# Performance work log

Hardware: AMD Instinct MI355X
Metric: run time of the kernel (lower is better)

The kernel has to match this reference:

```python
import jax, jax.numpy as jnp
import numpy as np

BIN_SIZE = 128
DIST_MULT = 0.1
LN_EPS = 1e-6


def setup_inputs() -> dict:
    key = jax.random.key(0)
    ks = jax.random.split(key, 24)
    B, N, D, DD, H = 8, 25600, 256, 128, 128
    s = 0.02
    inp = {
        'x': jax.random.normal(ks[0], (B, N, D), dtype=jnp.float32),
        'msk': jax.random.randint(ks[1], (B, N), 0, 2) > 0,
        'ln_g': jnp.ones((D,), jnp.float32),
        'ln_b': jnp.zeros((D,), jnp.float32),
        # ffn_dist: Linear(256,128) ELU Linear(128,128) ELU Linear(128,128)
        'w1': s * jax.random.normal(ks[2], (D, H), jnp.float32),
        'b1': jnp.zeros((H,), jnp.float32),
        'w2': s * jax.random.normal(ks[3], (H, H), jnp.float32),
        'b2': jnp.zeros((H,), jnp.float32),
        'w3': s * jax.random.normal(ks[4], (H, DD), jnp.float32),
        'b3': jnp.zeros((DD,), jnp.float32),
        # LSH codebook random rotations [distance_dim, max_num_bins//2]
        'codebook': jax.random.normal(ks[5], (DD, 100), jnp.float32),
        # two GHConvDense layers, hidden_dim=output_dim=256
        'theta0': jax.random.normal(ks[6], (D, D), jnp.float32) * s,
        'wh0': jax.random.normal(ks[7], (D, D), jnp.float32) * s,
        'wt0': jax.random.normal(ks[8], (D, D), jnp.float32) * s,
        'bt0': jnp.zeros((D,), jnp.float32),
        'theta1': jax.random.normal(ks[9], (D, D), jnp.float32) * s,
        'wh1': jax.random.normal(ks[10], (D, D), jnp.float32) * s,
        'wt1': jax.random.normal(ks[11], (D, D), jnp.float32) * s,
        'bt1': jnp.zeros((D,), jnp.float32),
    }
    return inp


def _forward(x, msk, ln_g, ln_b, w1, b1, w2, b2, w3, b3, codebook,
             theta0, wh0, wt0, bt0, theta1, wh1, wt1, bt1):
    B, n_elems, D = x.shape
    pad = (-n_elems) % BIN_SIZE  # static python int
    if pad:
        x = jnp.pad(x, ((0, 0), (0, pad), (0, 0)))
        msk = jnp.pad(msk, ((0, 0), (0, pad)), constant_values=True)
    Np = n_elems + pad
    n_bins = Np // BIN_SIZE

    # layernorm
    mu = jnp.mean(x, -1, keepdims=True)
    var = jnp.mean(jnp.square(x - mu), -1, keepdims=True)
    xn = (x - mu) * jax.lax.rsqrt(var + LN_EPS) * ln_g + ln_b

    # distance FFN + dist activation (elu)
    h = jax.nn.elu(xn @ w1 + b1)
    h = jax.nn.elu(h @ w2 + b2)
    x_dist = jax.nn.elu(h @ w3 + b3)  # [B, Np, distance_dim]

    # LSH binning
    mul = x_dist @ codebook[:, :max(1, n_bins // 2)]
    cmul = jnp.concatenate([mul, -mul], axis=-1)  # [B, Np, n_bins]
    a = jnp.argmax(cmul, axis=-1)
    bin_idx = a + jnp.where(msk, 0, n_bins - 1)
    bins_split = jnp.argsort(bin_idx, axis=-1)  # [B, Np]

    # gather into bins
    xm = jnp.take_along_axis(x_dist, bins_split[..., None], axis=1)
    xm = xm.reshape(B, n_bins, BIN_SIZE, x_dist.shape[-1])
    xb = jnp.take_along_axis(xn, bins_split[..., None], axis=1)
    xb = xb.reshape(B, n_bins, BIN_SIZE, D)
    mskf = jnp.take_along_axis(msk, bins_split, axis=1)
    mskf = mskf.reshape(B, n_bins, BIN_SIZE, 1).astype(x.dtype)

    # pairwise Gaussian kernel within each bin
    xk = xm * mskf
    nsq = jnp.sum(jnp.square(xk), -1)  # [B, nb, P]
    inner = jnp.einsum('bnpd,bnqd->bnpq', xk, xk)
    d2 = nsq[..., :, None] - 2.0 * inner + nsq[..., None, :]
    dist = jnp.sqrt(jnp.clip(d2, 1e-6, 1e6))
    dm = jnp.clip(jnp.exp(-DIST_MULT * dist), 0.0, 1.0)
    dm = dm * mskf * jnp.swapaxes(mskf, -1, -2)  # mask rows & cols [B,nb,P,P]

    # gated graph convolutions
    for th, wh, wt, bt in ((theta0, wh0, wt0, bt0), (theta1, wh1, wt1, bt1)):
        xmk = xb * mskf
        f_hom = jnp.einsum('bnpq,bnqd->bnpd', dm, (xmk @ th) * mskf)
        f_het = xmk @ wh
        gate = jax.nn.sigmoid(xb @ wt + bt)
        xb = jax.nn.elu(gate * f_hom + (1.0 - gate) * f_het) * mskf

    # reverse LSH scatter
    xb_flat = xb.reshape(B, Np, D)
    ret = jax.vmap(lambda idx, pts: jnp.zeros((Np, D), pts.dtype).at[idx].set(pts))(
        bins_split, xb_flat)
    return ret[:, :n_elems, :]


def reference(x, msk, ln_g, ln_b, w1, b1, w2, b2, w3, b3, codebook,
              theta0, wh0, wt0, bt0, theta1, wh1, wt1, bt1):
    return _forward(x, msk, ln_g, ln_b, w1, b1, w2, b2, w3, b3, codebook,
                    theta0, wh0, wt0, bt0, theta1, wh1, wt1, bt1)
```

## Files before the change

kernel.cpp:

```cpp
#include <hip/hip_runtime.h>
#include <math.h>

#define B_ 8
#define NP_ 25600
#define T_ (B_*NP_)
#define D_ 256
#define H_ 128
#define DD_ 128
#define NBINS_ 200
#define NIDS_ 400
#define PB_ 128
#define NC_ 100
#define GT_ (B_*NBINS_)

typedef __attribute__((ext_vector_type(8))) short bf16x8;
typedef __attribute__((ext_vector_type(4))) float f32x4;
typedef __attribute__((ext_vector_type(4))) unsigned short u16x4;
typedef unsigned short u16;

__device__ __forceinline__ float eluf(float v){ return v > 0.f ? v : expm1f(v); }
__device__ __forceinline__ u16 f2bf(float f){
  union { float f; unsigned u; } v; v.f = f;
  unsigned r = v.u + 0x7fffu + ((v.u >> 16) & 1u);
  return (u16)(r >> 16);
}
__device__ __forceinline__ float bf2f(u16 h){
  union { unsigned u; float f; } v; v.u = ((unsigned)h) << 16; return v.f;
}

__global__ void k_mask_detect(const unsigned int* __restrict__ m, int* __restrict__ flags){
  int any_f1 = 0, any_o = 0;
  for (int i = blockIdx.x*blockDim.x + threadIdx.x; i < T_/4; i += gridDim.x*blockDim.x){
    unsigned int w = m[i];
    if (w == 0x3F800000u) any_f1 = 1;
    else if (w > 1u) any_o = 1;
  }
  if (any_f1) atomicOr(&flags[0], 1);
  if (any_o)  atomicOr(&flags[1], 1);
}

__global__ void k_mask_convert(const void* __restrict__ m, const int* __restrict__ flags,
                               float* __restrict__ mskf){
  int i = blockIdx.x*256 + threadIdx.x;
  int mode = flags[0] ? 2 : (flags[1] ? 1 : 0);
  bool v;
  if (mode == 2)      v = ((const float*)m)[i] != 0.f;
  else if (mode == 1) v = ((const unsigned char*)m)[i] != 0;
  else                v = ((const int*)m)[i] != 0;
  mskf[i] = v ? 1.f : 0.f;
}

__global__ __launch_bounds__(256) void k_ln(const float* __restrict__ x,
    const float* __restrict__ g, const float* __restrict__ b, float* __restrict__ xn){
  const int wave = threadIdx.x >> 6, lane = threadIdx.x & 63;
  const long t = (long)blockIdx.x*4 + wave;
  float4 v = ((const float4*)(x + t*D_))[lane];
  float s  = v.x + v.y + v.z + v.w;
  float s2 = v.x*v.x + v.y*v.y + v.z*v.z + v.w*v.w;
  #pragma unroll
  for (int o = 32; o; o >>= 1){ s += __shfl_xor(s, o); s2 += __shfl_xor(s2, o); }
  const float mu = s * (1.f/D_);
  float var = s2*(1.f/D_) - mu*mu;
  var = fmaxf(var, 0.f);
  const float rs = rsqrtf(var + 1e-6f);
  float4 gg = ((const float4*)g)[lane];
  float4 bb = ((const float4*)b)[lane];
  float4 o4;
  o4.x = (v.x-mu)*rs*gg.x + bb.x;
  o4.y = (v.y-mu)*rs*gg.y + bb.y;
  o4.z = (v.z-mu)*rs*gg.z + bb.z;
  o4.w = (v.w-mu)*rs*gg.w + bb.w;
  ((float4*)(xn + t*D_))[lane] = o4;
}

template<int K>
__global__ __launch_bounds__(256) void k_gemm2(const float* __restrict__ A,
    const float* __restrict__ W, const float* __restrict__ bias, float* __restrict__ C){
  __shared__ __align__(16) float As[32*132];
  __shared__ __align__(16) float Bs[32*132];
  const size_t m0 = (size_t)blockIdx.x * 128;
  const int tid = threadIdx.x;
  const int tm = tid >> 4, tn = tid & 15;
  float acc[8][8] = {};
  for (int kc = 0; kc < K; kc += 32){
    __syncthreads();
    {
      const int r = tid >> 1, kq = (tid & 1) * 16;
      const float* src = &A[(m0 + r)*(size_t)K + kc + kq];
      #pragma unroll
      for (int q = 0; q < 4; ++q){
        const float4 v = ((const float4*)src)[q];
        As[(kq + q*4 + 0)*132 + r] = v.x;
        As[(kq + q*4 + 1)*132 + r] = v.y;
        As[(kq + q*4 + 2)*132 + r] = v.z;
        As[(kq + q*4 + 3)*132 + r] = v.w;
      }
      const int kk = tid >> 3, n0 = (tid & 7) * 16;
      const float* wsrc = &W[(size_t)(kc + kk)*128 + n0];
      #pragma unroll
      for (int q = 0; q < 4; ++q)
        *(float4*)&Bs[kk*132 + n0 + q*4] = ((const float4*)wsrc)[q];
    }
    __syncthreads();
    #pragma unroll
    for (int k = 0; k < 32; ++k){
      float a[8], b[8];
      *(float4*)&a[0] = *(const float4*)&As[k*132 + tm*8];
      *(float4*)&a[4] = *(const float4*)&As[k*132 + tm*8 + 4];
      *(float4*)&b[0] = *(const float4*)&Bs[k*132 + tn*8];
      *(float4*)&b[4] = *(const float4*)&Bs[k*132 + tn*8 + 4];
      #pragma unroll
      for (int i = 0; i < 8; ++i)
        #pragma unroll
        for (int j = 0; j < 8; ++j)
          acc[i][j] = fmaf(a[i], b[j], acc[i][j]);
    }
  }
  #pragma unroll
  for (int i = 0; i < 8; ++i){
    const size_t row = m0 + tm*8 + i;
    #pragma unroll
    for (int q = 0; q < 2; ++q){
      float4 o;
      o.x = eluf(acc[i][q*4+0] + bias[tn*8 + q*4+0]);
      o.y = eluf(acc[i][q*4+1] + bias[tn*8 + q*4+1]);
      o.z = eluf(acc[i][q*4+2] + bias[tn*8 + q*4+2]);
      o.w = eluf(acc[i][q*4+3] + bias[tn*8 + q*4+3]);
      *(float4*)&C[row*128 + tn*8 + q*4] = o;
    }
  }
}

__global__ void k_cbpad(const float* __restrict__ cb, float* __restrict__ cbp){
  const int k = blockIdx.x, c = threadIdx.x;
  cbp[k*128 + c] = (c < NC_) ? cb[k*NC_ + c] : 0.f;
}

__global__ __launch_bounds__(256) void k_mulmax(const float* __restrict__ A,
    const float* __restrict__ CB, const float* __restrict__ mskf, int* __restrict__ bidx){
  __shared__ __align__(16) float As[32*132];
  __shared__ __align__(16) float Bs[32*132];
  const size_t m0 = (size_t)blockIdx.x * 128;
  const int tid = threadIdx.x;
  const int tm = tid >> 4, tn = tid & 15;
  float acc[8][8] = {};
  for (int kc = 0; kc < DD_; kc += 32){
    __syncthreads();
    {
      const int r = tid >> 1, kq = (tid & 1) * 16;
      const float* src = &A[(m0 + r)*(size_t)DD_ + kc + kq];
      #pragma unroll
      for (int q = 0; q < 4; ++q){
        const float4 v = ((const float4*)src)[q];
        As[(kq + q*4 + 0)*132 + r] = v.x;
        As[(kq + q*4 + 1)*132 + r] = v.y;
        As[(kq + q*4 + 2)*132 + r] = v.z;
        As[(kq + q*4 + 3)*132 + r] = v.w;
      }
      const int kk = tid >> 3, n0 = (tid & 7) * 16;
      const float* wsrc = &CB[(size_t)(kc + kk)*128 + n0];
      #pragma unroll
      for (int q = 0; q < 4; ++q)
        *(float4*)&Bs[kk*132 + n0 + q*4] = ((const float4*)wsrc)[q];
    }
    __syncthreads();
    #pragma unroll
    for (int k = 0; k < 32; ++k){
      float a[8], b[8];
      *(float4*)&a[0] = *(const float4*)&As[k*132 + tm*8];
      *(float4*)&a[4] = *(const float4*)&As[k*132 + tm*8 + 4];
      *(float4*)&b[0] = *(const float4*)&Bs[k*132 + tn*8];
      *(float4*)&b[4] = *(const float4*)&Bs[k*132 + tn*8 + 4];
      #pragma unroll
      for (int i = 0; i < 8; ++i)
        #pragma unroll
        for (int j = 0; j < 8; ++j)
          acc[i][j] = fmaf(a[i], b[j], acc[i][j]);
    }
  }
  #pragma unroll
  for (int i = 0; i < 8; ++i){
    float bv = -1e30f; int bi = 0;
    #pragma unroll
    for (int j = 0; j < 8; ++j){
      const int c = tn*8 + j;
      if (c < NC_){
        const float v = acc[i][j];
        if (v > bv || (v == bv && c < bi)){ bv = v; bi = c; }
        const float nv = -v; const int nc2 = c + NC_;
        if (nv > bv || (nv == bv && nc2 < bi)){ bv = nv; bi = nc2; }
      }
    }
    #pragma unroll
    for (int o = 1; o < 16; o <<= 1){
      const float ov = __shfl_xor(bv, o);
      const int oi = __shfl_xor(bi, o);
      if (ov > bv || (ov == bv && oi < bi)){ bv = ov; bi = oi; }
    }
    if (tn == 0){
      const size_t t = m0 + tm*8 + i;
      bidx[t] = bi + (mskf[t] != 0.f ? 0 : NBINS_ - 1);
    }
  }
}

__global__ void k_hist(const int* __restrict__ bidx, int* __restrict__ hist){
  const int i = blockIdx.x*256 + threadIdx.x;
  const int b = i / NP_;
  atomicAdd(&hist[b*NIDS_ + bidx[i]], 1);
}

__global__ void k_prefix(const int* __restrict__ hist, int* __restrict__ offs){
  const int b = threadIdx.x;
  if (b < B_){
    int run = 0;
    for (int v = 0; v < NIDS_; ++v){ offs[b*NIDS_ + v] = run; run += hist[b*NIDS_ + v]; }
  }
}

__global__ __launch_bounds__(64) void k_binsort(const int* __restrict__ bidx,
    const int* __restrict__ offs, const int* __restrict__ hist, int* __restrict__ split){
  const int bv = blockIdx.x;
  if (hist[bv] == 0) return;
  const int b = bv / NIDS_, v = bv % NIDS_;
  int base = offs[bv];
  const int lane = threadIdx.x;
  const int* row = bidx + b*NP_;
  for (int i0 = 0; i0 < NP_; i0 += 64){
    const int i = i0 + lane;
    const bool m = (row[i] == v);
    const unsigned long long mk = __ballot(m);
    if (m){
      const int pos = base + __popcll(mk & ((1ull << lane) - 1ull));
      split[b*NP_ + pos] = i;
    }
    base += __popcll(mk);
  }
}

__global__ __launch_bounds__(256) void k_gather(const float* __restrict__ xn,
    const float* __restrict__ xd, const float* __restrict__ mskf,
    const int* __restrict__ split, u16* __restrict__ xmh,
    u16* __restrict__ xkh, float* __restrict__ mskg){
  const long j = (long)blockIdx.x*4 + (threadIdx.x >> 6);
  const int lane = threadIdx.x & 63;
  const int b = (int)(j / NP_);
  const int i = split[j];
  const long src = (long)b*NP_ + i;
  const float mv = mskf[src];
  const float4 v = ((const float4*)(xn + src*D_))[lane];
  u16x4 o;
  o[0] = f2bf(v.x*mv); o[1] = f2bf(v.y*mv); o[2] = f2bf(v.z*mv); o[3] = f2bf(v.w*mv);
  ((u16x4*)(xmh + j*D_))[lane] = o;
  if (lane < 32){
    const float4 w = ((const float4*)(xd + src*DD_))[lane];
    u16x4 ow;
    ow[0] = f2bf(w.x*mv); ow[1] = f2bf(w.y*mv); ow[2] = f2bf(w.z*mv); ow[3] = f2bf(w.w*mv);
    ((u16x4*)(xkh + j*DD_))[lane] = ow;
  }
  if (lane == 0) mskg[j] = mv;
}

__global__ __launch_bounds__(256) void k_wt(const float* __restrict__ W, u16* __restrict__ o){
  const int n = blockIdx.x, k = threadIdx.x;
  o[n*D_ + k] = f2bf(W[k*D_ + n]);
}
__global__ __launch_bounds__(256) void k_wt2(const float* __restrict__ wt,
    const float* __restrict__ wh, u16* __restrict__ o){
  const int n = blockIdx.x, k = threadIdx.x;
  const float v = (n < 256) ? wt[(size_t)k*D_ + n] : wh[(size_t)k*D_ + (n-256)];
  o[(size_t)n*D_ + k] = f2bf(v);
}

__device__ __forceinline__ void stage64(const u16* __restrict__ g, size_t row0,
    int ld, int k0, u16* Ls, int tid){
  #pragma unroll
  for (int s = 0; s < 4; ++s){
    const int r = (tid >> 3) + s*32, c8 = tid & 7;
    bf16x8 v = *(const bf16x8*)&g[(row0 + r)*(size_t)ld + k0 + c8*8];
    *(bf16x8*)&Ls[(r*8 + (c8 ^ (r & 7)))*8] = v;
  }
}
__device__ __forceinline__ void stage128(const u16* __restrict__ g, size_t row0,
    int ld, u16* Ls, int tid){
  #pragma unroll
  for (int s = 0; s < 8; ++s){
    const int r = (tid >> 4) + s*16, c8 = tid & 15;
    bf16x8 v = *(const bf16x8*)&g[(row0 + r)*(size_t)ld + c8*8];
    *(bf16x8*)&Ls[(r*16 + (c8 ^ (r & 7)))*8] = v;
  }
}
__device__ __forceinline__ bf16x8 ldf(const u16* Ls, int row, int c8, int ldc8){
  return *(const bf16x8*)&Ls[(row*ldc8 + (c8 ^ (row & 7)))*8];
}

__global__ __launch_bounds__(256) void k_dm(const u16* __restrict__ xk,
    const float* __restrict__ rm, u16* __restrict__ dmb){
  __shared__ __align__(16) u16 Xs[128*128];
  __shared__ float nsq[128];
  __shared__ float msl[128];
  const int g = blockIdx.x;
  const int tid = threadIdx.x, l = tid & 63, wid = tid >> 6;
  const int wr = wid >> 1, wc = wid & 1, lm = l & 15, lk = l >> 4;
  stage128(xk, (size_t)g*128, DD_, Xs, tid);
  if (tid < 128) msl[tid] = rm[(size_t)g*128 + tid];
  __syncthreads();
  f32x4 acc[4][4] = {};
  #pragma unroll
  for (int ks = 0; ks < 4; ++ks){
    bf16x8 a[4], b[4];
    #pragma unroll
    for (int mi = 0; mi < 4; ++mi) a[mi] = ldf(Xs, wr*64 + mi*16 + lm, ks*4 + lk, 16);
    #pragma unroll
    for (int ni = 0; ni < 4; ++ni) b[ni] = ldf(Xs, wc*64 + ni*16 + lm, ks*4 + lk, 16);
    #pragma unroll
    for (int mi = 0; mi < 4; ++mi)
      #pragma unroll
      for (int ni = 0; ni < 4; ++ni)
        acc[mi][ni] = __builtin_amdgcn_mfma_f32_16x16x32_bf16(a[mi], b[ni], acc[mi][ni], 0, 0, 0);
  }
  if (wr == wc && ((lm >> 2) == lk)){
    #pragma unroll
    for (int mi = 0; mi < 4; ++mi)
      nsq[wr*64 + mi*16 + lm] = acc[mi][mi][lm & 3];
  }
  __syncthreads();
  #pragma unroll
  for (int mi = 0; mi < 4; ++mi)
    #pragma unroll
    for (int ni = 0; ni < 4; ++ni)
      #pragma unroll
      for (int r = 0; r < 4; ++r){
        const int row = wr*64 + mi*16 + lk*4 + r;
        const int col = wc*64 + ni*16 + lm;
        float d2 = nsq[row] + nsq[col] - 2.f*acc[mi][ni][r];
        d2 = fminf(fmaxf(d2, 1e-6f), 1e6f);
        float w = expf(-0.1f * sqrtf(d2));
        w = fminf(w, 1.f);
        dmb[((size_t)g*PB_ + row)*PB_ + col] = f2bf(w * msl[row] * msl[col]);
      }
}

__global__ __launch_bounds__(256) void k_tmm(const u16* __restrict__ thT,
    const u16* __restrict__ X, u16* __restrict__ tT){
  __shared__ __align__(16) u16 As[128*64];
  __shared__ __align__(16) u16 Bs[128*64];
  const int g = blockIdx.x, h = blockIdx.y;
  const int tid = threadIdx.x, l = tid & 63, wid = tid >> 6;
  const int wr = wid >> 1, wc = wid & 1, lm = l & 15, lk = l >> 4;
  f32x4 acc[4][4] = {};
  for (int kt = 0; kt < 4; ++kt){
    if (kt) __syncthreads();
    stage64(thT, (size_t)h*128, D_, kt*64, As, tid);
    stage64(X,   (size_t)g*128, D_, kt*64, Bs, tid);
    __syncthreads();
    #pragma unroll
    for (int ks = 0; ks < 2; ++ks){
      bf16x8 a[4], b[4];
      #pragma unroll
      for (int mi = 0; mi < 4; ++mi) a[mi] = ldf(As, wr*64 + mi*16 + lm, ks*4 + lk, 8);
      #pragma unroll
      for (int ni = 0; ni < 4; ++ni) b[ni] = ldf(Bs, wc*64 + ni*16 + lm, ks*4 + lk, 8);
      #pragma unroll
      for (int mi = 0; mi < 4; ++mi)
        #pragma unroll
        for (int ni = 0; ni < 4; ++ni)
          acc[mi][ni] = __builtin_amdgcn_mfma_f32_16x16x32_bf16(a[mi], b[ni], acc[mi][ni], 0, 0, 0);
    }
  }
  #pragma unroll
  for (int mi = 0; mi < 4; ++mi)
    #pragma unroll
    for (int ni = 0; ni < 4; ++ni)
      #pragma unroll
      for (int r = 0; r < 4; ++r){
        const int row = wr*64 + mi*16 + lk*4 + r;
        const int col = wc*64 + ni*16 + lm;
        tT[((size_t)g*D_ + h*128 + row)*PB_ + col] = f2bf(acc[mi][ni][r]);
      }
}

__global__ __launch_bounds__(256) void k_gg(const u16* __restrict__ X,
    const u16* __restrict__ WT, u16* __restrict__ o){
  __shared__ __align__(16) u16 As[128*64];
  __shared__ __align__(16) u16 Bs[128*64];
  const int n0 = blockIdx.x * 128;
  const size_t r0 = (size_t)blockIdx.y * 128;
  const int tid = threadIdx.x, l = tid & 63, wid = tid >> 6;
  const int wr = wid >> 1, wc = wid & 1, lm = l & 15, lk = l >> 4;
  f32x4 acc[4][4] = {};
  for (int kt = 0; kt < 4; ++kt){
    if (kt) __syncthreads();
    stage64(X,  r0,          D_, kt*64, As, tid);
    stage64(WT, (size_t)n0,  D_, kt*64, Bs, tid);
    __syncthreads();
    #pragma unroll
    for (int ks = 0; ks < 2; ++ks){
      bf16x8 a[4], b[4];
      #pragma unroll
      for (int mi = 0; mi < 4; ++mi) a[mi] = ldf(As, wr*64 + mi*16 + lm, ks*4 + lk, 8);
      #pragma unroll
      for (int ni = 0; ni < 4; ++ni) b[ni] = ldf(Bs, wc*64 + ni*16 + lm, ks*4 + lk, 8);
      #pragma unroll
      for (int mi = 0; mi < 4; ++mi)
        #pragma unroll
        for (int ni = 0; ni < 4; ++ni)
          acc[mi][ni] = __builtin_amdgcn_mfma_f32_16x16x32_bf16(a[mi], b[ni], acc[mi][ni], 0, 0, 0);
    }
  }
  #pragma unroll
  for (int mi = 0; mi < 4; ++mi)
    #pragma unroll
    for (int ni = 0; ni < 4; ++ni)
      #pragma unroll
      for (int r = 0; r < 4; ++r){
        const int row = wr*64 + mi*16 + lk*4 + r;
        const int col = wc*64 + ni*16 + lm;
        o[(r0 + row)*512 + n0 + col] = f2bf(acc[mi][ni][r]);
      }
}

template<int OUT>
__global__ __launch_bounds__(256) void k_bmix(const u16* __restrict__ dmb,
    const u16* __restrict__ tT, const u16* __restrict__ atah,
    const float* __restrict__ btv, const int* __restrict__ split,
    u16* __restrict__ o16, float* __restrict__ o32){
  __shared__ __align__(16) u16 As[128*128];
  __shared__ __align__(16) u16 Bs[128*128];
  __shared__ int ssp[128];
  const int h = blockIdx.x, g = blockIdx.y;
  const int tid = threadIdx.x, l = tid & 63, wid = tid >> 6;
  const int wr = wid >> 1, wc = wid & 1, lm = l & 15, lk = l >> 4;
  stage128(dmb, (size_t)g*128, PB_, As, tid);
  stage128(tT, (size_t)g*D_ + h*128, PB_, Bs, tid);
  if (OUT){ if (tid < 128) ssp[tid] = split[g*128 + tid]; }
  __syncthreads();
  f32x4 acc[4][4] = {};
  #pragma unroll
  for (int ks = 0; ks < 4; ++ks){
    bf16x8 a[4], b[4];
    #pragma unroll
    for (int mi = 0; mi < 4; ++mi) a[mi] = ldf(As, wr*64 + mi*16 + lm, ks*4 + lk, 16);
    #pragma unroll
    for (int ni = 0; ni < 4; ++ni) b[ni] = ldf(Bs, wc*64 + ni*16 + lm, ks*4 + lk, 16);
    #pragma unroll
    for (int mi = 0; mi < 4; ++mi)
      #pragma unroll
      for (int ni = 0; ni < 4; ++ni)
        acc[mi][ni] = __builtin_amdgcn_mfma_f32_16x16x32_bf16(a[mi], b[ni], acc[mi][ni], 0, 0, 0);
  }
  __syncthreads();
  #pragma unroll
  for (int s = 0; s < 8; ++s){
    const int r = (tid >> 4) + s*16, c8 = tid & 15;
    const size_t gbase = ((size_t)g*128 + r)*512 + h*128 + c8*8;
    *(bf16x8*)&As[r*128 + c8*8] = *(const bf16x8*)&atah[gbase];
    *(bf16x8*)&Bs[r*128 + c8*8] = *(const bf16x8*)&atah[gbase + 256];
  }
  __syncthreads();
  #pragma unroll
  for (int mi = 0; mi < 4; ++mi)
    #pragma unroll
    for (int ni = 0; ni < 4; ++ni){
      const int colc = wc*64 + ni*16 + lm;
      const int gc = h*128 + colc;
      const float bb = btv[gc];
      #pragma unroll
      for (int r = 0; r < 4; ++r){
        const int row = wr*64 + mi*16 + lk*4 + r;
        const float at = bf2f(As[row*128 + colc]);
        const float ahv = bf2f(Bs[row*128 + colc]);
        const float gt = 1.f/(1.f + expf(-(at + bb)));
        const float o = eluf(gt*acc[mi][ni][r] + (1.f - gt)*ahv);
        if (OUT == 0){
          o16[((size_t)g*128 + row)*D_ + gc] = f2bf(o);
        } else {
          const int b = g / NBINS_;
          o32[((size_t)b*NP_ + ssp[row])*D_ + gc] = o;
        }
      }
    }
}

extern "C" void kernel_launch(void* const* d_in, const int* in_sizes, int n_in,
                              void* d_out, int out_size, void* d_ws, size_t ws_size,
                              hipStream_t stream){
  (void)in_sizes; (void)n_in; (void)out_size;
  const float* x    = (const float*)d_in[0];
  const void*  msk  = d_in[1];
  const float* ln_g = (const float*)d_in[2];
  const float* ln_b = (const float*)d_in[3];
  const float* w1 = (const float*)d_in[4];
  const float* b1 = (const float*)d_in[5];
  const float* w2 = (const float*)d_in[6];
  const float* b2 = (const float*)d_in[7];
  const float* w3 = (const float*)d_in[8];
  const float* b3 = (const float*)d_in[9];
  const float* cb = (const float*)d_in[10];
  const float* th0 = (const float*)d_in[11];
  const float* wh0 = (const float*)d_in[12];
  const float* wt0 = (const float*)d_in[13];
  const float* bt0 = (const float*)d_in[14];
  const float* th1 = (const float*)d_in[15];
  const float* wh1 = (const float*)d_in[16];
  const float* wt1 = (const float*)d_in[17];
  const float* bt1 = (const float*)d_in[18];
  float* out = (float*)d_out;

  char* ws = (char*)d_ws;
  size_t off = 0;
  auto alloc = [&](size_t bytes) -> void* {
    void* p = ws + off; off += (bytes + 255) & ~(size_t)255; return p;
  };
  int* flags = (int*)alloc(2*sizeof(int));
  int* hist  = (int*)alloc((size_t)B_*NIDS_*4);
  int* offs  = (int*)alloc((size_t)B_*NIDS_*4);
  int* bidx  = (int*)alloc((size_t)T_*4);
  int* split = (int*)alloc((size_t)T_*4);
  float* mskf = (float*)alloc((size_t)T_*4);
  float* mskg = (float*)alloc((size_t)T_*4);
  float* cbp = (float*)alloc((size_t)128*128*4);
  u16* thT0 = (u16*)alloc((size_t)D_*D_*2);
  u16* thT1 = (u16*)alloc((size_t)D_*D_*2);
  u16* wtwh0 = (u16*)alloc((size_t)512*D_*2);
  u16* wtwh1 = (u16*)alloc((size_t)512*D_*2);
  char* regA = (char*)alloc((size_t)T_*512*2);
  u16* xmh = (u16*)alloc((size_t)T_*D_*2);
  char* regC = (char*)alloc((size_t)T_*D_*2);
  u16* tT  = (u16*)alloc((size_t)T_*D_*2);
  u16* xb1 = (u16*)alloc((size_t)T_*D_*2);
  if (off > ws_size) return;

  float* P = (float*)regA;
  float* Q = P + (size_t)T_*DD_;
  u16* atah = (u16*)regA;
  u16* xkh = (u16*)regC;
  u16* dmb = xkh + (size_t)T_*DD_;
  float* xn = out;

  hipMemsetAsync(flags, 0, 2*sizeof(int), stream);
  hipMemsetAsync(hist, 0, (size_t)B_*NIDS_*4, stream);

  k_mask_detect<<<64, 256, 0, stream>>>((const unsigned int*)msk, flags);
  k_mask_convert<<<T_/256, 256, 0, stream>>>(msk, flags, mskf);

  k_ln<<<T_/4, 256, 0, stream>>>(x, ln_g, ln_b, xn);

  k_cbpad<<<128, 128, 0, stream>>>(cb, cbp);
  k_wt<<<256, 256, 0, stream>>>(th0, thT0);
  k_wt<<<256, 256, 0, stream>>>(th1, thT1);
  k_wt2<<<512, 256, 0, stream>>>(wt0, wh0, wtwh0);
  k_wt2<<<512, 256, 0, stream>>>(wt1, wh1, wtwh1);

  k_gemm2<D_><<<T_/128, 256, 0, stream>>>(xn, w1, b1, P);
  k_gemm2<H_><<<T_/128, 256, 0, stream>>>(P, w2, b2, Q);
  k_gemm2<H_><<<T_/128, 256, 0, stream>>>(Q, w3, b3, P);

  k_mulmax<<<T_/128, 256, 0, stream>>>(P, cbp, mskf, bidx);
  k_hist<<<T_/256, 256, 0, stream>>>(bidx, hist);
  k_prefix<<<1, 64, 0, stream>>>(hist, offs);
  k_binsort<<<B_*NIDS_, 64, 0, stream>>>(bidx, offs, hist, split);

  k_gather<<<T_/4, 256, 0, stream>>>(xn, P, mskf, split, xmh, xkh, mskg);
  k_dm<<<GT_, 256, 0, stream>>>(xkh, mskg, dmb);

  k_gg<<<dim3(4, T_/128), 256, 0, stream>>>(xmh, wtwh0, atah);
  k_tmm<<<dim3(GT_, 2), 256, 0, stream>>>(thT0, xmh, tT);
  k_bmix<0><<<dim3(2, GT_), 256, 0, stream>>>(dmb, tT, atah, bt0, nullptr, xb1, nullptr);

  k_gg<<<dim3(4, T_/128), 256, 0, stream>>>(xb1, wtwh1, atah);
  k_tmm<<<dim3(GT_, 2), 256, 0, stream>>>(thT1, xb1, tT);
  k_bmix<1><<<dim3(2, GT_), 256, 0, stream>>>(dmb, tT, atah, bt1, split, nullptr, out);
}
```

Before: 1.524 ms.

## Stage GEMM tiles with direct global-to-LDS loads and register-prefetch A tiles

Replaces register round-trip staging of shared-memory tiles with global_load_lds direct copies across the bf16 MFMA kernels and the fp32 GEMMs, keeping the XOR swizzle by permuting source addresses instead of destination slots. In the fp32 GEMM and codebook kernels, the A tile is prefetched into registers one k-chunk ahead so the global load overlaps the FMA loop, and the B tile loses its padding. This is meant to cut VGPR pressure and load-store instruction count during staging. The risk is that the unpadded B layout causes LDS bank conflicts and that the direct loads need correct waits before the barrier.

```diff
diff --git a/kernel.cpp b/kernel.cpp
--- a/kernel.cpp
+++ b/kernel.cpp
@@ -26,6 +26,11 @@
 }
 __device__ __forceinline__ float bf2f(u16 h){
   union { unsigned u; float f; } v; v.u = ((unsigned)h) << 16; return v.f;
+}
+
+__device__ __forceinline__ void gl16(void* lds, const void* g){
+  __builtin_amdgcn_global_load_lds((const __attribute__((address_space(1))) void*)g,
+                                   (__attribute__((address_space(3))) void*)lds, 16, 0, 0);
 }
 
 __global__ void k_mask_detect(const unsigned int* __restrict__ m, int* __restrict__ flags){
@@ -77,38 +82,47 @@
 __global__ __launch_bounds__(256) void k_gemm2(const float* __restrict__ A,
     const float* __restrict__ W, const float* __restrict__ bias, float* __restrict__ C){
   __shared__ __align__(16) float As[32*132];
-  __shared__ __align__(16) float Bs[32*132];
+  __shared__ __align__(16) float Bs[32*128];
   const size_t m0 = (size_t)blockIdx.x * 128;
   const int tid = threadIdx.x;
   const int tm = tid >> 4, tn = tid & 15;
+  const int w = tid >> 6, l = tid & 63;
+  const int ar = tid >> 1, akq = (tid & 1) * 16;
   float acc[8][8] = {};
+  float4 pre[4];
+  {
+    const float* src = &A[(m0 + ar)*(size_t)K + akq];
+    #pragma unroll
+    for (int q = 0; q < 4; ++q) pre[q] = ((const float4*)src)[q];
+  }
   for (int kc = 0; kc < K; kc += 32){
+    if (kc) __syncthreads();
+    #pragma unroll
+    for (int q = 0; q < 4; ++q){
+      As[(akq + q*4 + 0)*132 + ar] = pre[q].x;
+      As[(akq + q*4 + 1)*132 + ar] = pre[q].y;
+      As[(akq + q*4 + 2)*132 + ar] = pre[q].z;
+      As[(akq + q*4 + 3)*132 + ar] = pre[q].w;
+    }
+    #pragma unroll
+    for (int s = 0; s < 4; ++s){
+      const int G = (s*4 + w)*64 + l;
+      const int r = G >> 5, c4 = G & 31;
+      gl16(&Bs[G*4], &W[(size_t)(kc + r)*128 + c4*4]);
+    }
     __syncthreads();
-    {
-      const int r = tid >> 1, kq = (tid & 1) * 16;
-      const float* src = &A[(m0 + r)*(size_t)K + kc + kq];
-      #pragma unroll
-      for (int q = 0; q < 4; ++q){
-        const float4 v = ((const float4*)src)[q];
-        As[(kq + q*4 + 0)*132 + r] = v.x;
-        As[(kq + q*4 + 1)*132 + r] = v.y;
-        As[(kq + q*4 + 2)*132 + r] = v.z;
-        As[(kq + q*4 + 3)*132 + r] = v.w;
-      }
-      const int kk = tid >> 3, n0 = (tid & 7) * 16;
-      const float* wsrc = &W[(size_t)(kc + kk)*128 + n0];
-      #pragma unroll
-      for (int q = 0; q < 4; ++q)
-        *(float4*)&Bs[kk*132 + n0 + q*4] = ((const float4*)wsrc)[q];
-    }
-    __syncthreads();
+    if (kc + 32 < K){
+      const float* src = &A[(m0 + ar)*(size_t)K + kc + 32 + akq];
+      #pragma unroll
+      for (int q = 0; q < 4; ++q) pre[q] = ((const float4*)src)[q];
+    }
     #pragma unroll
     for (int k = 0; k < 32; ++k){
       float a[8], b[8];
       *(float4*)&a[0] = *(const float4*)&As[k*132 + tm*8];
       *(float4*)&a[4] = *(const float4*)&As[k*132 + tm*8 + 4];
-      *(float4*)&b[0] = *(const float4*)&Bs[k*132 + tn*8];
-      *(float4*)&b[4] = *(const float4*)&Bs[k*132 + tn*8 + 4];
+      *(float4*)&b[0] = *(const float4*)&Bs[k*128 + tn*8];
+      *(float4*)&b[4] = *(const float4*)&Bs[k*128 + tn*8 + 4];
       #pragma unroll
       for (int i = 0; i < 8; ++i)
         #pragma unroll
@@ -139,38 +153,47 @@
 __global__ __launch_bounds__(256) void k_mulmax(const float* __restrict__ A,
     const float* __restrict__ CB, const float* __restrict__ mskf, int* __restrict__ bidx){
   __shared__ __align__(16) float As[32*132];
-  __shared__ __align__(16) float Bs[32*132];
+  __shared__ __align__(16) float Bs[32*128];
   const size_t m0 = (size_t)blockIdx.x * 128;
   const int tid = threadIdx.x;
   const int tm = tid >> 4, tn = tid & 15;
+  const int w = tid >> 6, l = tid & 63;
+  const int ar = tid >> 1, akq = (tid & 1) * 16;
   float acc[8][8] = {};
+  float4 pre[4];
+  {
+    const float* src = &A[(m0 + ar)*(size_t)DD_ + akq];
+    #pragma unroll
+    for (int q = 0; q < 4; ++q) pre[q] = ((const float4*)src)[q];
+  }
   for (int kc = 0; kc < DD_; kc += 32){
+    if (kc) __syncthreads();
+    #pragma unroll
+    for (int q = 0; q < 4; ++q){
+      As[(akq + q*4 + 0)*132 + ar] = pre[q].x;
+      As[(akq + q*4 + 1)*132 + ar] = pre[q].y;
+      As[(akq + q*4 + 2)*132 + ar] = pre[q].z;
+      As[(akq + q*4 + 3)*132 + ar] = pre[q].w;
+    }
+    #pragma unroll
+    for (int s = 0; s < 4; ++s){
+      const int G = (s*4 + w)*64 + l;
+      const int r = G >> 5, c4 = G & 31;
+      gl16(&Bs[G*4], &CB[(size_t)(kc + r)*128 + c4*4]);
+    }
     __syncthreads();
-    {
-      const int r = tid >> 1, kq = (tid & 1) * 16;
-      const float* src = &A[(m0 + r)*(size_t)DD_ + kc + kq];
-      #pragma unroll
-      for (int q = 0; q < 4; ++q){
-        const float4 v = ((const float4*)src)[q];
-        As[(kq + q*4 + 0)*132 + r] = v.x;
-        As[(kq + q*4 + 1)*132 + r] = v.y;
-        As[(kq + q*4 + 2)*132 + r] = v.z;
-        As[(kq + q*4 + 3)*132 + r] = v.w;
-      }
-      const int kk = tid >> 3, n0 = (tid & 7) * 16;
-      const float* wsrc = &CB[(size_t)(kc + kk)*128 + n0];
-      #pragma unroll
-      for (int q = 0; q < 4; ++q)
-        *(float4*)&Bs[kk*132 + n0 + q*4] = ((const float4*)wsrc)[q];
-    }
-    __syncthreads();
+    if (kc + 32 < DD_){
+      const float* src = &A[(m0 + ar)*(size_t)DD_ + kc + 32 + akq];
+      #pragma unroll
+      for (int q = 0; q < 4; ++q) pre[q] = ((const float4*)src)[q];
+    }
     #pragma unroll
     for (int k = 0; k < 32; ++k){
       float a[8], b[8];
       *(float4*)&a[0] = *(const float4*)&As[k*132 + tm*8];
       *(float4*)&a[4] = *(const float4*)&As[k*132 + tm*8 + 4];
-      *(float4*)&b[0] = *(const float4*)&Bs[k*132 + tn*8];
-      *(float4*)&b[4] = *(const float4*)&Bs[k*132 + tn*8 + 4];
+      *(float4*)&b[0] = *(const float4*)&Bs[k*128 + tn*8];
+      *(float4*)&b[4] = *(const float4*)&Bs[k*128 + tn*8 + 4];
       #pragma unroll
       for (int i = 0; i < 8; ++i)
         #pragma unroll
@@ -253,9 +276,9 @@
   o[0] = f2bf(v.x*mv); o[1] = f2bf(v.y*mv); o[2] = f2bf(v.z*mv); o[3] = f2bf(v.w*mv);
   ((u16x4*)(xmh + j*D_))[lane] = o;
   if (lane < 32){
-    const float4 w = ((const float4*)(xd + src*DD_))[lane];
+    const float4 ww = ((const float4*)(xd + src*DD_))[lane];
     u16x4 ow;
-    ow[0] = f2bf(w.x*mv); ow[1] = f2bf(w.y*mv); ow[2] = f2bf(w.z*mv); ow[3] = f2bf(w.w*mv);
+    ow[0] = f2bf(ww.x*mv); ow[1] = f2bf(ww.y*mv); ow[2] = f2bf(ww.z*mv); ow[3] = f2bf(ww.w*mv);
     ((u16x4*)(xkh + j*DD_))[lane] = ow;
   }
   if (lane == 0) mskg[j] = mv;
@@ -272,22 +295,24 @@
   o[(size_t)n*D_ + k] = f2bf(v);
 }
 
-__device__ __forceinline__ void stage64(const u16* __restrict__ g, size_t row0,
+__device__ __forceinline__ void stage64a(const u16* __restrict__ g, size_t row0,
     int ld, int k0, u16* Ls, int tid){
+  const int w = tid >> 6, l = tid & 63;
   #pragma unroll
   for (int s = 0; s < 4; ++s){
-    const int r = (tid >> 3) + s*32, c8 = tid & 7;
-    bf16x8 v = *(const bf16x8*)&g[(row0 + r)*(size_t)ld + k0 + c8*8];
-    *(bf16x8*)&Ls[(r*8 + (c8 ^ (r & 7)))*8] = v;
-  }
-}
-__device__ __forceinline__ void stage128(const u16* __restrict__ g, size_t row0,
+    const int G = (s*4 + w)*64 + l;
+    const int r = G >> 3, c8 = G & 7;
+    gl16(&Ls[G*8], &g[(row0 + r)*(size_t)ld + k0 + ((c8 ^ (r & 7))*8)]);
+  }
+}
+__device__ __forceinline__ void stage128a(const u16* __restrict__ g, size_t row0,
     int ld, u16* Ls, int tid){
+  const int w = tid >> 6, l = tid & 63;
   #pragma unroll
   for (int s = 0; s < 8; ++s){
-    const int r = (tid >> 4) + s*16, c8 = tid & 15;
-    bf16x8 v = *(const bf16x8*)&g[(row0 + r)*(size_t)ld + c8*8];
-    *(bf16x8*)&Ls[(r*16 + (c8 ^ (r & 7)))*8] = v;
+    const int G = (s*4 + w)*64 + l;
+    const int r = G >> 4, c8 = G & 15;
+    gl16(&Ls[G*8], &g[(row0 + r)*(size_t)ld + ((c8 ^ (r & 7))*8)]);
   }
 }
 __device__ __forceinline__ bf16x8 ldf(const u16* Ls, int row, int c8, int ldc8){
@@ -302,7 +327,7 @@
   const int g = blockIdx.x;
   const int tid = threadIdx.x, l = tid & 63, wid = tid >> 6;
   const int wr = wid >> 1, wc = wid & 1, lm = l & 15, lk = l >> 4;
-  stage128(xk, (size_t)g*128, DD_, Xs, tid);
+  stage128a(xk, (size_t)g*128, DD_, Xs, tid);
   if (tid < 128) msl[tid] = rm[(size_t)g*128 + tid];
   __syncthreads();
   f32x4 acc[4][4] = {};
@@ -351,8 +376,8 @@
   f32x4 acc[4][4] = {};
   for (int kt = 0; kt < 4; ++kt){
     if (kt) __syncthreads();
-    stage64(thT, (size_t)h*128, D_, kt*64, As, tid);
-    stage64(X,   (size_t)g*128, D_, kt*64, Bs, tid);
+    stage64a(thT, (size_t)h*128, D_, kt*64, As, tid);
+    stage64a(X,   (size_t)g*128, D_, kt*64, Bs, tid);
     __syncthreads();
     #pragma unroll
     for (int ks = 0; ks < 2; ++ks){
@@ -391,8 +416,8 @@
   f32x4 acc[4][4] = {};
   for (int kt = 0; kt < 4; ++kt){
     if (kt) __syncthreads();
-    stage64(X,  r0,          D_, kt*64, As, tid);
-    stage64(WT, (size_t)n0,  D_, kt*64, Bs, tid);
+    stage64a(X,  r0,          D_, kt*64, As, tid);
+    stage64a(WT, (size_t)n0,  D_, kt*64, Bs, tid);
     __syncthreads();
     #pragma unroll
     for (int ks = 0; ks < 2; ++ks){
@@ -431,8 +456,8 @@
   const int h = blockIdx.x, g = blockIdx.y;
   const int tid = threadIdx.x, l = tid & 63, wid = tid >> 6;
   const int wr = wid >> 1, wc = wid & 1, lm = l & 15, lk = l >> 4;
-  stage128(dmb, (size_t)g*128, PB_, As, tid);
-  stage128(tT, (size_t)g*D_ + h*128, PB_, Bs, tid);
+  stage128a(dmb, (size_t)g*128, PB_, As, tid);
+  stage128a(tT, (size_t)g*D_ + h*128, PB_, Bs, tid);
   if (OUT){ if (tid < 128) ssp[tid] = split[g*128 + tid]; }
   __syncthreads();
   f32x4 acc[4][4] = {};
@@ -450,12 +475,16 @@
         acc[mi][ni] = __builtin_amdgcn_mfma_f32_16x16x32_bf16(a[mi], b[ni], acc[mi][ni], 0, 0, 0);
   }
   __syncthreads();
-  #pragma unroll
-  for (int s = 0; s < 8; ++s){
-    const int r = (tid >> 4) + s*16, c8 = tid & 15;
-    const size_t gbase = ((size_t)g*128 + r)*512 + h*128 + c8*8;
-    *(bf16x8*)&As[r*128 + c8*8] = *(const bf16x8*)&atah[gbase];
-    *(bf16x8*)&Bs[r*128 + c8*8] = *(const bf16x8*)&atah[gbase + 256];
+  {
+    const int w = tid >> 6, ll = tid & 63;
+    #pragma unroll
+    for (int s = 0; s < 8; ++s){
+      const int G = (s*4 + w)*64 + ll;
+      const int r = G >> 4, c8 = G & 15;
+      const size_t gbase = ((size_t)g*128 + r)*512 + h*128 + c8*8;
+      gl16(&As[G*8], &atah[gbase]);
+      gl16(&Bs[G*8], &atah[gbase + 256]);
+    }
   }
   __syncthreads();
   #pragma unroll
```

After: 1.556 ms. 2.1% more time.

## Fuse theta GEMM into bin-mix kernel and stage tiles via direct global-to-LDS loads

Applied to the files above, without the earlier changes.

Removes the separate k_tmm kernel and its tT intermediate. Each k_tbmix block now computes its 128x128 slice of theta^T·X in registers, writes it swizzled into LDS, and immediately multiplies by the distance matrix. This eliminates a full write and read of a T×256 bf16 buffer and two launches. Separately, tile staging now uses global_load_lds, with the XOR swizzle moved to the global address side, so data skips the register round trip. In exchange, the fused kernel does more serial work per block and uses more LDS.

```diff
diff --git a/kernel.cpp b/kernel.cpp
--- a/kernel.cpp
+++ b/kernel.cpp
@@ -26,6 +26,11 @@
 }
 __device__ __forceinline__ float bf2f(u16 h){
   union { unsigned u; float f; } v; v.u = ((unsigned)h) << 16; return v.f;
+}
+
+__device__ __forceinline__ void gl16(void* lds, const void* g){
+  __builtin_amdgcn_global_load_lds((const __attribute__((address_space(1))) void*)g,
+                                   (__attribute__((address_space(3))) void*)lds, 16, 0, 0);
 }
 
 __global__ void k_mask_detect(const unsigned int* __restrict__ m, int* __restrict__ flags){
@@ -253,9 +258,9 @@
   o[0] = f2bf(v.x*mv); o[1] = f2bf(v.y*mv); o[2] = f2bf(v.z*mv); o[3] = f2bf(v.w*mv);
   ((u16x4*)(xmh + j*D_))[lane] = o;
   if (lane < 32){
-    const float4 w = ((const float4*)(xd + src*DD_))[lane];
+    const float4 ww = ((const float4*)(xd + src*DD_))[lane];
     u16x4 ow;
-    ow[0] = f2bf(w.x*mv); ow[1] = f2bf(w.y*mv); ow[2] = f2bf(w.z*mv); ow[3] = f2bf(w.w*mv);
+    ow[0] = f2bf(ww.x*mv); ow[1] = f2bf(ww.y*mv); ow[2] = f2bf(ww.z*mv); ow[3] = f2bf(ww.w*mv);
     ((u16x4*)(xkh + j*DD_))[lane] = ow;
   }
   if (lane == 0) mskg[j] = mv;
@@ -272,22 +277,24 @@
   o[(size_t)n*D_ + k] = f2bf(v);
 }
 
-__device__ __forceinline__ void stage64(const u16* __restrict__ g, size_t row0,
+__device__ __forceinline__ void stage64a(const u16* __restrict__ g, size_t row0,
     int ld, int k0, u16* Ls, int tid){
+  const int w = tid >> 6, l = tid & 63;
   #pragma unroll
   for (int s = 0; s < 4; ++s){
-    const int r = (tid >> 3) + s*32, c8 = tid & 7;
-    bf16x8 v = *(const bf16x8*)&g[(row0 + r)*(size_t)ld + k0 + c8*8];
-    *(bf16x8*)&Ls[(r*8 + (c8 ^ (r & 7)))*8] = v;
-  }
-}
-__device__ __forceinline__ void stage128(const u16* __restrict__ g, size_t row0,
+    const int G = (s*4 + w)*64 + l;
+    const int r = G >> 3, c8 = G & 7;
+    gl16(&Ls[G*8], &g[(row0 + r)*(size_t)ld + k0 + ((c8 ^ (r & 7))*8)]);
+  }
+}
+__device__ __forceinline__ void stage128a(const u16* __restrict__ g, size_t row0,
     int ld, u16* Ls, int tid){
+  const int w = tid >> 6, l = tid & 63;
   #pragma unroll
   for (int s = 0; s < 8; ++s){
-    const int r = (tid >> 4) + s*16, c8 = tid & 15;
-    bf16x8 v = *(const bf16x8*)&g[(row0 + r)*(size_t)ld + c8*8];
-    *(bf16x8*)&Ls[(r*16 + (c8 ^ (r & 7)))*8] = v;
+    const int G = (s*4 + w)*64 + l;
+    const int r = G >> 4, c8 = G & 15;
+    gl16(&Ls[G*8], &g[(row0 + r)*(size_t)ld + ((c8 ^ (r & 7))*8)]);
   }
 }
 __device__ __forceinline__ bf16x8 ldf(const u16* Ls, int row, int c8, int ldc8){
@@ -302,7 +309,7 @@
   const int g = blockIdx.x;
   const int tid = threadIdx.x, l = tid & 63, wid = tid >> 6;
   const int wr = wid >> 1, wc = wid & 1, lm = l & 15, lk = l >> 4;
-  stage128(xk, (size_t)g*128, DD_, Xs, tid);
+  stage128a(xk, (size_t)g*128, DD_, Xs, tid);
   if (tid < 128) msl[tid] = rm[(size_t)g*128 + tid];
   __syncthreads();
   f32x4 acc[4][4] = {};
@@ -338,45 +345,6 @@
         float w = expf(-0.1f * sqrtf(d2));
         w = fminf(w, 1.f);
         dmb[((size_t)g*PB_ + row)*PB_ + col] = f2bf(w * msl[row] * msl[col]);
-      }
-}
-
-__global__ __launch_bounds__(256) void k_tmm(const u16* __restrict__ thT,
-    const u16* __restrict__ X, u16* __restrict__ tT){
-  __shared__ __align__(16) u16 As[128*64];
-  __shared__ __align__(16) u16 Bs[128*64];
-  const int g = blockIdx.x, h = blockIdx.y;
-  const int tid = threadIdx.x, l = tid & 63, wid = tid >> 6;
-  const int wr = wid >> 1, wc = wid & 1, lm = l & 15, lk = l >> 4;
-  f32x4 acc[4][4] = {};
-  for (int kt = 0; kt < 4; ++kt){
-    if (kt) __syncthreads();
-    stage64(thT, (size_t)h*128, D_, kt*64, As, tid);
-    stage64(X,   (size_t)g*128, D_, kt*64, Bs, tid);
-    __syncthreads();
-    #pragma unroll
-    for (int ks = 0; ks < 2; ++ks){
-      bf16x8 a[4], b[4];
-      #pragma unroll
-      for (int mi = 0; mi < 4; ++mi) a[mi] = ldf(As, wr*64 + mi*16 + lm, ks*4 + lk, 8);
-      #pragma unroll
-      for (int ni = 0; ni < 4; ++ni) b[ni] = ldf(Bs, wc*64 + ni*16 + lm, ks*4 + lk, 8);
-      #pragma unroll
-      for (int mi = 0; mi < 4; ++mi)
-        #pragma unroll
-        for (int ni = 0; ni < 4; ++ni)
-          acc[mi][ni] = __builtin_amdgcn_mfma_f32_16x16x32_bf16(a[mi], b[ni], acc[mi][ni], 0, 0, 0);
-    }
-  }
-  #pragma unroll
-  for (int mi = 0; mi < 4; ++mi)
-    #pragma unroll
-    for (int ni = 0; ni < 4; ++ni)
-      #pragma unroll
-      for (int r = 0; r < 4; ++r){
-        const int row = wr*64 + mi*16 + lk*4 + r;
-        const int col = wc*64 + ni*16 + lm;
-        tT[((size_t)g*D_ + h*128 + row)*PB_ + col] = f2bf(acc[mi][ni][r]);
       }
 }
 
@@ -391,8 +359,8 @@
   f32x4 acc[4][4] = {};
   for (int kt = 0; kt < 4; ++kt){
     if (kt) __syncthreads();
-    stage64(X,  r0,          D_, kt*64, As, tid);
-    stage64(WT, (size_t)n0,  D_, kt*64, Bs, tid);
+    stage64a(X,  r0,          D_, kt*64, As, tid);
+    stage64a(WT, (size_t)n0,  D_, kt*64, Bs, tid);
     __syncthreads();
     #pragma unroll
     for (int ks = 0; ks < 2; ++ks){
@@ -421,28 +389,60 @@
 }
 
 template<int OUT>
-__global__ __launch_bounds__(256) void k_bmix(const u16* __restrict__ dmb,
-    const u16* __restrict__ tT, const u16* __restrict__ atah,
-    const float* __restrict__ btv, const int* __restrict__ split,
-    u16* __restrict__ o16, float* __restrict__ o32){
-  __shared__ __align__(16) u16 As[128*128];
-  __shared__ __align__(16) u16 Bs[128*128];
+__global__ __launch_bounds__(256) void k_tbmix(const u16* __restrict__ dmb,
+    const u16* __restrict__ thT, const u16* __restrict__ X,
+    const u16* __restrict__ atah, const float* __restrict__ btv,
+    const int* __restrict__ split, u16* __restrict__ o16, float* __restrict__ o32){
+  __shared__ __align__(16) u16 bufA[128*128];
+  __shared__ __align__(16) u16 bufB[128*128];
   __shared__ int ssp[128];
   const int h = blockIdx.x, g = blockIdx.y;
   const int tid = threadIdx.x, l = tid & 63, wid = tid >> 6;
   const int wr = wid >> 1, wc = wid & 1, lm = l & 15, lk = l >> 4;
-  stage128(dmb, (size_t)g*128, PB_, As, tid);
-  stage128(tT, (size_t)g*D_ + h*128, PB_, Bs, tid);
+  u16* SA = bufA;
+  u16* SB = bufA + 128*64;
   if (OUT){ if (tid < 128) ssp[tid] = split[g*128 + tid]; }
+  f32x4 acc1[4][4] = {};
+  for (int kt = 0; kt < 4; ++kt){
+    if (kt) __syncthreads();
+    stage64a(thT, (size_t)h*128, D_, kt*64, SA, tid);
+    stage64a(X,   (size_t)g*128, D_, kt*64, SB, tid);
+    __syncthreads();
+    #pragma unroll
+    for (int ks = 0; ks < 2; ++ks){
+      bf16x8 a[4], b[4];
+      #pragma unroll
+      for (int mi = 0; mi < 4; ++mi) a[mi] = ldf(SA, wr*64 + mi*16 + lm, ks*4 + lk, 8);
+      #pragma unroll
+      for (int ni = 0; ni < 4; ++ni) b[ni] = ldf(SB, wc*64 + ni*16 + lm, ks*4 + lk, 8);
+      #pragma unroll
+      for (int mi = 0; mi < 4; ++mi)
+        #pragma unroll
+        for (int ni = 0; ni < 4; ++ni)
+          acc1[mi][ni] = __builtin_amdgcn_mfma_f32_16x16x32_bf16(a[mi], b[ni], acc1[mi][ni], 0, 0, 0);
+    }
+  }
+  __syncthreads();
+  #pragma unroll
+  for (int mi = 0; mi < 4; ++mi)
+    #pragma unroll
+    for (int ni = 0; ni < 4; ++ni)
+      #pragma unroll
+      for (int r = 0; r < 4; ++r){
+        const int row = wr*64 + mi*16 + lk*4 + r;
+        const int col = wc*64 + ni*16 + lm;
+        bufB[(row*16 + ((col >> 3) ^ (row & 7)))*8 + (col & 7)] = f2bf(acc1[mi][ni][r]);
+      }
+  stage128a(dmb, (size_t)g*128, PB_, bufA, tid);
   __syncthreads();
   f32x4 acc[4][4] = {};
   #pragma unroll
   for (int ks = 0; ks < 4; ++ks){
     bf16x8 a[4], b[4];
     #pragma unroll
-    for (int mi = 0; mi < 4; ++mi) a[mi] = ldf(As, wr*64 + mi*16 + lm, ks*4 + lk, 16);
-    #pragma unroll
-    for (int ni = 0; ni < 4; ++ni) b[ni] = ldf(Bs, wc*64 + ni*16 + lm, ks*4 + lk, 16);
+    for (int mi = 0; mi < 4; ++mi) a[mi] = ldf(bufA, wr*64 + mi*16 + lm, ks*4 + lk, 16);
+    #pragma unroll
+    for (int ni = 0; ni < 4; ++ni) b[ni] = ldf(bufB, wc*64 + ni*16 + lm, ks*4 + lk, 16);
     #pragma unroll
     for (int mi = 0; mi < 4; ++mi)
       #pragma unroll
@@ -450,12 +450,16 @@
         acc[mi][ni] = __builtin_amdgcn_mfma_f32_16x16x32_bf16(a[mi], b[ni], acc[mi][ni], 0, 0, 0);
   }
   __syncthreads();
-  #pragma unroll
-  for (int s = 0; s < 8; ++s){
-    const int r = (tid >> 4) + s*16, c8 = tid & 15;
-    const size_t gbase = ((size_t)g*128 + r)*512 + h*128 + c8*8;
-    *(bf16x8*)&As[r*128 + c8*8] = *(const bf16x8*)&atah[gbase];
-    *(bf16x8*)&Bs[r*128 + c8*8] = *(const bf16x8*)&atah[gbase + 256];
+  {
+    const int w = tid >> 6, ll = tid & 63;
+    #pragma unroll
+    for (int s = 0; s < 8; ++s){
+      const int G = (s*4 + w)*64 + ll;
+      const int r = G >> 4, c8 = G & 15;
+      const size_t gbase = ((size_t)g*128 + r)*512 + h*128 + c8*8;
+      gl16(&bufA[G*8], &atah[gbase]);
+      gl16(&bufB[G*8], &atah[gbase + 256]);
+    }
   }
   __syncthreads();
   #pragma unroll
@@ -468,8 +472,8 @@
       #pragma unroll
       for (int r = 0; r < 4; ++r){
         const int row = wr*64 + mi*16 + lk*4 + r;
-        const float at = bf2f(As[row*128 + colc]);
-        const float ahv = bf2f(Bs[row*128 + colc]);
+        const float at = bf2f(bufA[row*128 + colc]);
+        const float ahv = bf2f(bufB[row*128 + colc]);
         const float gt = 1.f/(1.f + expf(-(at + bb)));
         const float o = eluf(gt*acc[mi][ni][r] + (1.f - gt)*ahv);
         if (OUT == 0){
@@ -527,7 +531,6 @@
   char* regA = (char*)alloc((size_t)T_*512*2);
   u16* xmh = (u16*)alloc((size_t)T_*D_*2);
   char* regC = (char*)alloc((size_t)T_*D_*2);
-  u16* tT  = (u16*)alloc((size_t)T_*D_*2);
   u16* xb1 = (u16*)alloc((size_t)T_*D_*2);
   if (off > ws_size) return;
 
@@ -565,10 +568,8 @@
   k_dm<<<GT_, 256, 0, stream>>>(xkh, mskg, dmb);
 
   k_gg<<<dim3(4, T_/128), 256, 0, stream>>>(xmh, wtwh0, atah);
-  k_tmm<<<dim3(GT_, 2), 256, 0, stream>>>(thT0, xmh, tT);
-  k_bmix<0><<<dim3(2, GT_), 256, 0, stream>>>(dmb, tT, atah, bt0, nullptr, xb1, nullptr);
+  k_tbmix<0><<<dim3(2, GT_), 256, 0, stream>>>(dmb, thT0, xmh, atah, bt0, nullptr, xb1, nullptr);
 
   k_gg<<<dim3(4, T_/128), 256, 0, stream>>>(xb1, wtwh1, atah);
-  k_tmm<<<dim3(GT_, 2), 256, 0, stream>>>(thT1, xb1, tT);
-  k_bmix<1><<<dim3(2, GT_), 256, 0, stream>>>(dmb, tT, atah, bt1, split, nullptr, out);
-}
+  k_tbmix<1><<<dim3(2, GT_), 256, 0, stream>>>(dmb, thT1, xb1, atah, bt1, split, nullptr, out);
+}
```

Result: faster. 1.440 ms (-5.5%).
